# Kernel tuning notes

Hardware: AMD Instinct MI355X
Metric: run time of the kernel (lower is better)

The kernel has to match this reference:

```python
import jax, jax.numpy as jnp
import numpy as np
import math

B, S, D = 4, 2048, 1024
N_HEADS = 16
D_FF = 4096
T_DIM = 256
KEEP_RATIO = 0.7
EPS = 1e-5


def _layernorm(x):
    mu = jnp.mean(x, axis=-1, keepdims=True)
    var = jnp.mean((x - mu) ** 2, axis=-1, keepdims=True)
    return (x - mu) * jax.lax.rsqrt(var + EPS)


def _ada_ln(x, cond, W, b):
    # cond: (B, T_DIM); W: (2D, T_DIM)
    p = jax.nn.silu(cond) @ W.T + b            # (B, 2D)
    gamma, beta = jnp.split(p, 2, axis=-1)
    return _layernorm(x) * (1.0 + gamma[:, None, :]) + beta[:, None, :]


def _mha(h, in_w, in_b, out_w, out_b):
    b, s, d = h.shape
    hd = d // N_HEADS
    qkv = h @ in_w.T + in_b                     # (b, s, 3d)
    q, k, v = jnp.split(qkv, 3, axis=-1)
    def heads(t):
        return t.reshape(b, s, N_HEADS, hd).transpose(0, 2, 1, 3)
    q, k, v = heads(q), heads(k), heads(v)
    scores = jnp.einsum('bhqd,bhkd->bhqk', q, k) / math.sqrt(hd)
    attn = jax.nn.softmax(scores, axis=-1)
    o = jnp.einsum('bhqk,bhkd->bhqd', attn, v)  # (b, h, s, hd)
    o = o.transpose(0, 2, 1, 3).reshape(b, s, d)
    return o @ out_w.T + out_b


def setup_inputs() -> dict:
    key = jax.random.key(0)
    ks = jax.random.split(key, 24)
    sc = 0.02
    return {
        'x': jax.random.normal(ks[0], (B, S, D), jnp.float32),
        't_emb': jax.random.normal(ks[1], (B, T_DIM), jnp.float32),
        'tr_w1': jax.random.normal(ks[2], (32, D), jnp.float32) * sc,
        'tr_b1': jnp.zeros((32,), jnp.float32),
        'tr_w2': jax.random.normal(ks[3], (1, 32), jnp.float32) * sc,
        'tr_b2': jnp.zeros((1,), jnp.float32),
        'ln1_w': jax.random.normal(ks[4], (2 * D, T_DIM), jnp.float32) * sc,
        'ln1_b': jnp.zeros((2 * D,), jnp.float32),
        'ln2_w': jax.random.normal(ks[5], (2 * D, T_DIM), jnp.float32) * sc,
        'ln2_b': jnp.zeros((2 * D,), jnp.float32),
        'in_proj_w': jax.random.normal(ks[6], (3 * D, D), jnp.float32) * sc,
        'in_proj_b': jnp.zeros((3 * D,), jnp.float32),
        'out_w': jax.random.normal(ks[7], (D, D), jnp.float32) * sc,
        'out_b': jnp.zeros((D,), jnp.float32),
        'ffn_w1': jax.random.normal(ks[8], (D_FF, D), jnp.float32) * sc,
        'ffn_b1': jnp.zeros((D_FF,), jnp.float32),
        'ffn_w2': jax.random.normal(ks[9], (D, D_FF), jnp.float32) * sc,
        'ffn_b2': jnp.zeros((D,), jnp.float32),
        # torch inits gates to zero; use small randn so the block is non-trivial
        'gate_attn': jax.random.normal(ks[10], (1, 1, D), jnp.float32) * sc,
        'gate_ffn': jax.random.normal(ks[11], (1, 1, D), jnp.float32) * sc,
    }


def reference(x, t_emb, tr_w1, tr_b1, tr_w2, tr_b2, ln1_w, ln1_b, ln2_w, ln2_b,
              in_proj_w, in_proj_b, out_w, out_b, ffn_w1, ffn_b1, ffn_w2, ffn_b2,
              gate_attn, gate_ffn):
    b, s, d = x.shape
    num_keep = max(int(s * KEEP_RATIO), 1)

    # token importance on detached x (stop_gradient mirrors x.detach())
    xd = jax.lax.stop_gradient(x)
    imp = jax.nn.silu(xd @ tr_w1.T + tr_b1) @ tr_w2.T + tr_b2  # (b, s, 1)
    imp = imp[..., 0]
    _, idx = jax.lax.top_k(imp, num_keep)
    idx = jnp.sort(idx, axis=-1)                               # (b, num_keep)

    x_sel = jnp.take_along_axis(x, idx[..., None], axis=1)     # (b, k, d)

    h = _ada_ln(x_sel, t_emb, ln1_w, ln1_b)
    h = _mha(h, in_proj_w, in_proj_b, out_w, out_b)
    x_sel = x_sel + gate_attn * h

    h = _ada_ln(x_sel, t_emb, ln2_w, ln2_b)
    h = jax.nn.gelu(h @ ffn_w1.T + ffn_b1, approximate=False) @ ffn_w2.T + ffn_b2
    x_sel = x_sel + gate_ffn * h

    batch_idx = jnp.arange(b)[:, None]
    return x.at[batch_idx, idx].set(x_sel)
```

## Files before the change

### kernel.cpp

```cpp
#include <hip/hip_runtime.h>
#include <hip/hip_bf16.h>
#include <cmath>
#include <cstdint>

typedef __bf16 bf16;
typedef __bf16 bf16x8 __attribute__((ext_vector_type(8)));
typedef __bf16 bf16x4 __attribute__((ext_vector_type(4)));
typedef float  f32x4  __attribute__((ext_vector_type(4)));

constexpr int B_   = 4;
constexpr int S_   = 2048;
constexpr int D_   = 1024;
constexpr int H_   = 16;
constexpr int DFF_ = 4096;
constexpr int TD_  = 256;
constexpr int KEEP = 1433;
constexpr int M_TOT = B_ * KEEP;
constexpr int MPAD  = 5888;
constexpr int QT64  = (KEEP + 63) / 64;
constexpr int NKV   = (KEEP + 63) / 64;
constexpr float EPS = 1e-5f;
constexpr float QSCALE = 0.18033688011112042f;

__device__ __forceinline__ f32x4 mfma16(bf16x8 a, bf16x8 b, f32x4 c) {
  return __builtin_amdgcn_mfma_f32_16x16x32_bf16(a, b, c, 0, 0, 0);
}

#define GLOAD_LDS(gp, lp)                                                     \
  __builtin_amdgcn_global_load_lds(                                           \
      (const __attribute__((address_space(1))) void*)(gp),                    \
      (__attribute__((address_space(3))) void*)(lp), 16, 0, 0)

__global__ __launch_bounds__(256) void k_impgemv(
    const float* __restrict__ x, const float* __restrict__ w1,
    double* __restrict__ hidden)
{
  const int lane = threadIdx.x & 63, w = threadIdx.x >> 6;
  const int tok0 = blockIdx.x * 16 + w * 4;
  const int u0 = blockIdx.y * 8;
  const float* xb = x + (size_t)tok0 * D_ + lane * 4;
  const float* wb = w1 + (size_t)u0 * D_ + lane * 4;
  double acc[4][8] = {};
#pragma unroll 2
  for (int c = 0; c < D_; c += 256) {
    float4 xv[4], wv[8];
#pragma unroll
    for (int i = 0; i < 4; ++i)
      xv[i] = *(const float4*)(xb + (size_t)i * D_ + c);
#pragma unroll
    for (int u = 0; u < 8; ++u)
      wv[u] = *(const float4*)(wb + (size_t)u * D_ + c);
#pragma unroll
    for (int i = 0; i < 4; ++i)
#pragma unroll
      for (int u = 0; u < 8; ++u) {
        acc[i][u] += (double)xv[i].x * (double)wv[u].x;
        acc[i][u] += (double)xv[i].y * (double)wv[u].y;
        acc[i][u] += (double)xv[i].z * (double)wv[u].z;
        acc[i][u] += (double)xv[i].w * (double)wv[u].w;
      }
  }
#pragma unroll
  for (int i = 0; i < 4; ++i)
#pragma unroll
    for (int u = 0; u < 8; ++u) {
      double s = acc[i][u];
      for (int o = 32; o > 0; o >>= 1) s += __shfl_xor(s, o);
      acc[i][u] = s;
    }
  if (lane == 0) {
#pragma unroll
    for (int i = 0; i < 4; ++i)
#pragma unroll
      for (int u = 0; u < 8; ++u)
        hidden[(size_t)(tok0 + i) * 32 + u0 + u] = acc[i][u];
  }
}

__global__ __launch_bounds__(256) void k_imptail(
    const double* __restrict__ hidden, const float* __restrict__ b1,
    const float* __restrict__ w2, const float* __restrict__ b2,
    double* __restrict__ imp)
{
  const int tok = blockIdx.x * 256 + threadIdx.x;
  const double* hp = hidden + (size_t)tok * 32;
  double r = 0.0;
#pragma unroll
  for (int u = 0; u < 32; ++u) {
    double s = hp[u] + (double)b1[u];
    double sv = s / (1.0 + exp(-s));
    r += sv * (double)w2[u];
  }
  imp[tok] = r + (double)b2[0];
}

__global__ __launch_bounds__(256) void k_rank(const double* __restrict__ imp,
                                              int* __restrict__ rank)
{
  const int b = blockIdx.x >> 5;
  const int seg = blockIdx.x & 31;
  __shared__ double vals[S_];
  const double* ib = imp + (size_t)b * S_;
  for (int i = threadIdx.x; i < S_ / 2; i += 256)
    ((double2*)vals)[i] = ((const double2*)ib)[i];
  __syncthreads();
  const int tl = threadIdx.x >> 2;
  const int part = threadIdx.x & 3;
  const int s = seg * 64 + tl;
  const double v = vals[s];
  int cnt = 0;
  for (int j = part * 512; j < (part + 1) * 512; ++j) {
    double u = vals[j];
    cnt += (u > v) || (u == v && j < s);
  }
  cnt += __shfl_xor(cnt, 1);
  cnt += __shfl_xor(cnt, 2);
  if (part == 0) rank[b * S_ + s] = cnt;
}

__global__ __launch_bounds__(256) void k_compact(const int* __restrict__ rank,
                                                 int* __restrict__ idx)
{
  const int b = blockIdx.x;
  __shared__ int wcnt[4];
  __shared__ int base_s;
  if (threadIdx.x == 0) base_s = 0;
  __syncthreads();
  const int t = threadIdx.x, lane = t & 63, w = t >> 6;
  for (int c = 0; c < S_ / 256; ++c) {
    const int s = c * 256 + t;
    const bool kept = rank[b * S_ + s] < KEEP;
    unsigned long long m = __ballot(kept);
    int piw = __popcll(m & ((1ull << lane) - 1ull));
    if (lane == 0) wcnt[w] = __popcll(m);
    __syncthreads();
    int off = base_s;
    for (int i = 0; i < w; ++i) off += wcnt[i];
    if (kept) idx[b * KEEP + off + piw] = s;
    __syncthreads();
    if (t == 0) base_s += wcnt[0] + wcnt[1] + wcnt[2] + wcnt[3];
    __syncthreads();
  }
}

__global__ __launch_bounds__(256) void k_condproj(
    const float* __restrict__ temb, const float* __restrict__ W,
    const float* __restrict__ bias, float* __restrict__ p)
{
  const int gw = (int)((blockIdx.x * 256 + threadIdx.x) >> 6);
  const int lane = threadIdx.x & 63;
  const int b = gw >> 11;
  const int row = gw & 2047;
  const float* te = temb + (size_t)b * TD_;
  const float* wr = W + (size_t)row * TD_;
  float acc = 0.f;
  for (int i = lane; i < TD_; i += 64) {
    float c = te[i];
    acc += (c / (1.f + __expf(-c))) * wr[i];
  }
  for (int o = 32; o > 0; o >>= 1) acc += __shfl_down(acc, o);
  if (lane == 0) p[(size_t)b * 2 * D_ + row] = acc + bias[row];
}

__global__ void k_f2b(const float* __restrict__ src, bf16* __restrict__ dst, int n4)
{
  int i = blockIdx.x * 256 + threadIdx.x;
  if (i < n4) {
    float4 v = ((const float4*)src)[i];
    bf16x4 o = {(bf16)v.x, (bf16)v.y, (bf16)v.z, (bf16)v.w};
    ((bf16x4*)dst)[i] = o;
  }
}

__global__ __launch_bounds__(256) void k_adaln(
    const float* __restrict__ xsrc, const int* __restrict__ idx,
    const float* __restrict__ p, bf16* __restrict__ hout)
{
  const int r = blockIdx.x, t = threadIdx.x;
  bf16* orow = hout + (size_t)r * D_;
  if (r >= M_TOT) {
    bf16x4 z = {(bf16)0.f, (bf16)0.f, (bf16)0.f, (bf16)0.f};
    ((bf16x4*)orow)[t] = z;
    return;
  }
  const int b = r / KEEP, j = r - b * KEEP;
  const int s = idx[b * KEEP + j];
  const float* xr = xsrc + ((size_t)(b * S_ + s)) * D_;
  float4 v = ((const float4*)xr)[t];
  __shared__ float red[8];
  float sum = v.x + v.y + v.z + v.w;
  for (int o = 32; o > 0; o >>= 1) sum += __shfl_down(sum, o);
  const int lane = t & 63, w = t >> 6;
  if (lane == 0) red[w] = sum;
  __syncthreads();
  const float mu = (red[0] + red[1] + red[2] + red[3]) * (1.f / D_);
  const float dx = v.x - mu, dy = v.y - mu, dz = v.z - mu, dw = v.w - mu;
  float vs = dx * dx + dy * dy + dz * dz + dw * dw;
  for (int o = 32; o > 0; o >>= 1) vs += __shfl_down(vs, o);
  if (lane == 0) red[4 + w] = vs;
  __syncthreads();
  const float rstd = rsqrtf((red[4] + red[5] + red[6] + red[7]) * (1.f / D_) + EPS);
  const float* gp = p + (size_t)b * 2 * D_;
  float4 g  = ((const float4*)gp)[t];
  float4 be = ((const float4*)(gp + D_))[t];
  bf16x4 o;
  o[0] = (bf16)(dx * rstd * (1.f + g.x) + be.x);
  o[1] = (bf16)(dy * rstd * (1.f + g.y) + be.y);
  o[2] = (bf16)(dz * rstd * (1.f + g.z) + be.z);
  o[3] = (bf16)(dw * rstd * (1.f + g.w) + be.w);
  ((bf16x4*)orow)[t] = o;
}

template <int BN, int MODE>
__global__ __launch_bounds__(256) void k_gemm(
    const bf16* __restrict__ A, const bf16* __restrict__ W,
    const float* __restrict__ bias, bf16* __restrict__ Cbf,
    const float* __restrict__ gate, const int* __restrict__ idx,
    float* __restrict__ resid, int N, int K, int gn)
{
  constexpr int WN = BN / 2;
  constexpr int NJ = WN / 16;
  __shared__ bf16 As[2][128 * 64];
  __shared__ bf16 Ws[2][BN * 64];
  const int t = threadIdx.x, lane = t & 63;
  const int w = t >> 6, wr = w >> 1, wc = w & 1;
  const int fr = lane & 15, fq = lane >> 4;

  const int nwg = gridDim.x, orig = blockIdx.x;
  const int q8 = nwg >> 3, r8 = nwg & 7;
  const int xc = orig & 7, pos = orig >> 3;
  const int wgid = (xc < r8 ? xc * (q8 + 1) : r8 * (q8 + 1) + (xc - r8) * q8) + pos;
  const int bm = wgid / gn, bn = wgid - bm * gn;

  const bf16* Ab = A + (size_t)bm * 128 * K;
  const bf16* Wb = W + (size_t)bn * BN * K;

  auto stage = [&](int buf, int kt) {
    const int ko = kt * 64;
#pragma unroll
    for (int it = 0; it < 4; ++it) {
      const int e = it * 256 + t;
      const int row = e >> 3, pc = e & 7;
      const int lc = pc ^ (row & 7);
      GLOAD_LDS(Ab + (size_t)row * K + ko + lc * 8, &As[buf][0] + e * 8);
    }
#pragma unroll
    for (int it = 0; it < BN / 32; ++it) {
      const int e = it * 256 + t;
      const int row = e >> 3, pc = e & 7;
      const int lc = pc ^ (row & 7);
      GLOAD_LDS(Wb + (size_t)row * K + ko + lc * 8, &Ws[buf][0] + e * 8);
    }
  };

  f32x4 acc[4][NJ] = {};
  stage(0, 0);
  const int nkt = K >> 6;
  int cur = 0;
  for (int kt = 0; kt < nkt; ++kt) {
    __syncthreads();
    if (kt + 1 < nkt) stage(cur ^ 1, kt + 1);
    const char* Al = (const char*)&As[cur][0];
    const char* Wl = (const char*)&Ws[cur][0];
#pragma unroll
    for (int kk = 0; kk < 2; ++kk) {
      bf16x8 af[4], wf[NJ];
#pragma unroll
      for (int i = 0; i < 4; ++i)
        af[i] = *(const bf16x8*)(Al + (wr * 64 + i * 16 + fr) * 128 +
                                 (((kk * 4 + fq) ^ (fr & 7)) << 4));
#pragma unroll
      for (int j = 0; j < NJ; ++j)
        wf[j] = *(const bf16x8*)(Wl + (wc * WN + j * 16 + fr) * 128 +
                                 (((kk * 4 + fq) ^ (fr & 7)) << 4));
#pragma unroll
      for (int i = 0; i < 4; ++i)
#pragma unroll
        for (int j = 0; j < NJ; ++j)
          acc[i][j] = mfma16(af[i], wf[j], acc[i][j]);
    }
    cur ^= 1;
  }

#pragma unroll
  for (int i = 0; i < 4; ++i) {
#pragma unroll
    for (int j = 0; j < NJ; ++j) {
#pragma unroll
      for (int r = 0; r < 4; ++r) {
        const int m = bm * 128 + wr * 64 + i * 16 + fq * 4 + r;
        const int n = bn * BN + wc * WN + j * 16 + fr;
        float v = acc[i][j][r] + bias[n];
        if (MODE == 0) {
          if (n < D_) v *= QSCALE;
          Cbf[(size_t)m * N + n] = (bf16)v;
        } else if (MODE == 1) {
          float gl = 0.5f * v * (1.f + erff(v * 0.70710678118654752f));
          Cbf[(size_t)m * N + n] = (bf16)gl;
        } else {
          if (m < M_TOT) {
            const int b = m / KEEP, jj = m - b * KEEP;
            const int s = idx[b * KEEP + jj];
            resid[((size_t)(b * S_ + s)) * D_ + n] += gate[n] * v;
          }
        }
      }
    }
  }
}

__global__ __launch_bounds__(256) void k_attn(const bf16* __restrict__ qkv,
                                              bf16* __restrict__ out)
{
  __shared__ bf16 Klds[2][64 * 64];
  __shared__ bf16 Vlds[2][64 * 64];

  const int t = threadIdx.x;
  const int lane = t & 63, w = t >> 6;
  const int fr = lane & 15, fq = lane >> 4;
  const int qt = blockIdx.x, h = blockIdx.y, b = blockIdx.z;
  const size_t rowbase = (size_t)b * KEEP;
  const size_t RS = 3 * D_;
  const bf16* kbase = qkv + rowbase * RS + D_ + h * 64;
  const bf16* vbase = qkv + rowbase * RS + 2 * D_ + h * 64;

  const int wq0 = qt * 64 + w * 16;
  const int qrow = min(wq0 + fr, KEEP - 1);
  const bf16* qp = qkv + (rowbase + qrow) * RS + h * 64 + fq * 8;
  const bf16x8 qf0 = *(const bf16x8*)qp;
  const bf16x8 qf1 = *(const bf16x8*)(qp + 32);

  f32x4 o[4] = {};
  float mrow = -INFINITY, lrow = 0.f;

  const int p0 = t, p1 = 256 + t;
  auto kaddr = [&](int p, int kv) {
    const int row = p >> 3, c8p = p & 7;
    const int c8 = c8p ^ ((row & 7) ^ (row >> 3));
    const int gr = min(kv + row, KEEP - 1);
    return kbase + (size_t)gr * RS + c8 * 8;
  };
  auto vaddr = [&](int p, int kv) {
    const int db = p >> 7, ksub = (p >> 3) & 15, jr = (p >> 1) & 3,
              c8lo = p & 1;
    const int vrow = ksub * 4 + jr, vc8 = db * 2 + c8lo;
    const int gr = min(kv + vrow, KEEP - 1);
    return vbase + (size_t)gr * RS + vc8 * 8;
  };
  const bf16* kp0 = kaddr(p0, 0);
  const bf16* kp1 = kaddr(p1, 0);
  const bf16* vp0 = vaddr(p0, 0);
  const bf16* vp1 = vaddr(p1, 0);

  auto stage_fast = [&](int buf) {
    GLOAD_LDS(kp0, &Klds[buf][0] + p0 * 8);
    GLOAD_LDS(kp1, &Klds[buf][0] + p1 * 8);
    GLOAD_LDS(vp0, &Vlds[buf][0] + p0 * 8);
    GLOAD_LDS(vp1, &Vlds[buf][0] + p1 * 8);
    kp0 += 64 * RS; kp1 += 64 * RS; vp0 += 64 * RS; vp1 += 64 * RS;
  };
  auto stage_last = [&](int buf, int kv) {
    GLOAD_LDS(kaddr(p0, kv), &Klds[buf][0] + p0 * 8);
    GLOAD_LDS(kaddr(p1, kv), &Klds[buf][0] + p1 * 8);
    GLOAD_LDS(vaddr(p0, kv), &Vlds[buf][0] + p0 * 8);
    GLOAD_LDS(vaddr(p1, kv), &Vlds[buf][0] + p1 * 8);
  };

  stage_fast(0);
  int cur = 0;

  const unsigned vbase_lds0 =
      (unsigned)(size_t)(__attribute__((address_space(3))) bf16*)&Vlds[0][0];
  const unsigned vbase_lds1 =
      (unsigned)(size_t)(__attribute__((address_space(3))) bf16*)&Vlds[1][0];

  for (int ti = 0; ti < NKV; ++ti) {
    const int kv = ti * 64;
    __syncthreads();
    if (ti < NKV - 2) stage_fast(cur ^ 1);
    else if (ti == NKV - 2) stage_last(cur ^ 1, kv + 64);

    const char* Kl = (const char*)&Klds[cur][0];

    f32x4 sc[4];
    __builtin_amdgcn_s_setprio(1);
#pragma unroll
    for (int f = 0; f < 4; ++f) {
      const int row = ((f >> 1) << 5) + ((fr >> 2) << 3) + ((f & 1) << 1) +
                      (fr & 1) + (((fr >> 1) & 1) << 2);
      const int swz = (row & 7) ^ (row >> 3);
      const bf16x8 kf0 = *(const bf16x8*)(Kl + row * 128 + ((fq ^ swz) << 4));
      const bf16x8 kf1 =
          *(const bf16x8*)(Kl + row * 128 + (((fq ^ 4) ^ swz) << 4));
      f32x4 s = {0.f, 0.f, 0.f, 0.f};
      s = mfma16(kf0, qf0, s);
      s = mfma16(kf1, qf1, s);
      sc[f] = s;
    }
    __builtin_amdgcn_s_setprio(0);

    if (ti == NKV - 1) {
#pragma unroll
      for (int f = 0; f < 4; ++f)
#pragma unroll
        for (int r = 0; r < 4; ++r) {
          const int kl = ((f >> 1) << 5) + (fq << 3) + ((f & 1) << 1) +
                         (r & 1) + ((r >> 1) << 2);
          if (kv + kl >= KEEP) sc[f][r] = -INFINITY;
        }
    }
    float mx = sc[0][0];
#pragma unroll
    for (int f = 0; f < 4; ++f)
#pragma unroll
      for (int r = 0; r < 4; ++r) mx = fmaxf(mx, sc[f][r]);
    mx = fmaxf(mx, __shfl_xor(mx, 16));
    mx = fmaxf(mx, __shfl_xor(mx, 32));

    const bool noresc = __all(mx <= mrow + 8.f);
    const float mnew = noresc ? mrow : fmaxf(mrow, mx);
    float ps = 0.f;
    bf16 pe[4][4];
#pragma unroll
    for (int f = 0; f < 4; ++f)
#pragma unroll
      for (int r = 0; r < 4; ++r) {
        const float pv = exp2f(sc[f][r] - mnew);
        ps += pv;
        pe[f][r] = (bf16)pv;
      }
    ps += __shfl_xor(ps, 16);
    ps += __shfl_xor(ps, 32);
    if (!noresc) {
      const float fac = exp2f(mrow - mnew);
      lrow *= fac;
#pragma unroll
      for (int db = 0; db < 4; ++db) {
        o[db][0] *= fac; o[db][1] *= fac; o[db][2] *= fac; o[db][3] *= fac;
      }
      mrow = mnew;
    }
    lrow += ps;

    const bf16x8 pb[2] = {
        {pe[0][0], pe[0][1], pe[1][0], pe[1][1],
         pe[0][2], pe[0][3], pe[1][2], pe[1][3]},
        {pe[2][0], pe[2][1], pe[3][0], pe[3][1],
         pe[2][2], pe[2][3], pe[3][2], pe[3][3]}};
    const unsigned vb =
        (cur ? vbase_lds1 : vbase_lds0) + ((unsigned)fq << 7);
#pragma unroll
    for (int c = 0; c < 2; ++c) {
      const unsigned addr = vb + c * 1024;
      bf16x4 t0, t1, t2, t3, t4, t5, t6, t7;
      asm volatile(
          "ds_read_b64_tr_b16 %0, %8 offset:0\n\t"
          "ds_read_b64_tr_b16 %1, %8 offset:128\n\t"
          "ds_read_b64_tr_b16 %2, %8 offset:2048\n\t"
          "ds_read_b64_tr_b16 %3, %8 offset:2176\n\t"
          "ds_read_b64_tr_b16 %4, %8 offset:4096\n\t"
          "ds_read_b64_tr_b16 %5, %8 offset:4224\n\t"
          "ds_read_b64_tr_b16 %6, %8 offset:6144\n\t"
          "ds_read_b64_tr_b16 %7, %8 offset:6272\n\t"
          "s_waitcnt lgkmcnt(0)"
          : "=&v"(t0), "=&v"(t1), "=&v"(t2), "=&v"(t3),
            "=&v"(t4), "=&v"(t5), "=&v"(t6), "=&v"(t7)
          : "v"(addr));
      const bf16x8 vf0 = __builtin_shufflevector(t0, t1, 0, 1, 2, 3, 4, 5, 6, 7);
      const bf16x8 vf1 = __builtin_shufflevector(t2, t3, 0, 1, 2, 3, 4, 5, 6, 7);
      const bf16x8 vf2 = __builtin_shufflevector(t4, t5, 0, 1, 2, 3, 4, 5, 6, 7);
      const bf16x8 vf3 = __builtin_shufflevector(t6, t7, 0, 1, 2, 3, 4, 5, 6, 7);
      __builtin_amdgcn_s_setprio(1);
      o[0] = mfma16(vf0, pb[c], o[0]);
      o[1] = mfma16(vf1, pb[c], o[1]);
      o[2] = mfma16(vf2, pb[c], o[2]);
      o[3] = mfma16(vf3, pb[c], o[3]);
      __builtin_amdgcn_s_setprio(0);
    }
    cur ^= 1;
  }

  const int q = wq0 + fr;
  if (q < KEEP) {
    const float inv = 1.f / lrow;
#pragma unroll
    for (int db = 0; db < 4; ++db) {
      bf16x4 wv = {(bf16)(o[db][0] * inv), (bf16)(o[db][1] * inv),
                   (bf16)(o[db][2] * inv), (bf16)(o[db][3] * inv)};
      *(bf16x4*)(out + (rowbase + q) * (size_t)D_ + h * 64 + db * 16 + fq * 4) =
          wv;
    }
  }
}

extern "C" void kernel_launch(void* const* d_in, const int* in_sizes, int n_in,
                              void* d_out, int out_size, void* d_ws, size_t ws_size,
                              hipStream_t stream)
{
  (void)in_sizes; (void)n_in; (void)out_size; (void)ws_size;
  const float* x      = (const float*)d_in[0];
  const float* t_emb  = (const float*)d_in[1];
  const float* tr_w1  = (const float*)d_in[2];
  const float* tr_b1  = (const float*)d_in[3];
  const float* tr_w2  = (const float*)d_in[4];
  const float* tr_b2  = (const float*)d_in[5];
  const float* ln1_w  = (const float*)d_in[6];
  const float* ln1_b  = (const float*)d_in[7];
  const float* ln2_w  = (const float*)d_in[8];
  const float* ln2_b  = (const float*)d_in[9];
  const float* in_w   = (const float*)d_in[10];
  const float* in_b   = (const float*)d_in[11];
  const float* out_w  = (const float*)d_in[12];
  const float* out_b  = (const float*)d_in[13];
  const float* f1_w   = (const float*)d_in[14];
  const float* f1_b   = (const float*)d_in[15];
  const float* f2_w   = (const float*)d_in[16];
  const float* f2_b   = (const float*)d_in[17];
  const float* gate_a = (const float*)d_in[18];
  const float* gate_f = (const float*)d_in[19];

  char* ws = (char*)d_ws;
  size_t off = 0;
  auto alloc = [&](size_t bytes) -> char* {
    char* p = ws + off;
    off = (off + bytes + 255) & ~(size_t)255;
    return p;
  };
  double* imp  = (double*)alloc((size_t)B_ * S_ * 8);
  double* hid  = (double*)alloc((size_t)B_ * S_ * 32 * 8);
  int* rank    = (int*)alloc((size_t)B_ * S_ * 4);
  int* idx     = (int*)alloc((size_t)B_ * KEEP * 4);
  float* p1    = (float*)alloc((size_t)B_ * 2 * D_ * 4);
  float* p2    = (float*)alloc((size_t)B_ * 2 * D_ * 4);
  bf16* w_in   = (bf16*)alloc((size_t)3 * D_ * D_ * 2);
  bf16* w_out  = (bf16*)alloc((size_t)D_ * D_ * 2);
  bf16* w_f1   = (bf16*)alloc((size_t)DFF_ * D_ * 2);
  bf16* w_f2   = (bf16*)alloc((size_t)D_ * DFF_ * 2);
  bf16* h_bf   = (bf16*)alloc((size_t)MPAD * D_ * 2);
  bf16* big    = (bf16*)alloc((size_t)MPAD * (3 * D_ + D_) * 2);
  bf16* qkv    = big;
  bf16* attn   = big + (size_t)MPAD * 3 * D_;
  bf16* ffn1   = big;

  hipMemcpyAsync(d_out, x, (size_t)B_ * S_ * D_ * 4, hipMemcpyDeviceToDevice, stream);

  k_impgemv<<<dim3(B_ * S_ / 16, 4), 256, 0, stream>>>(x, tr_w1, hid);
  k_imptail<<<B_ * S_ / 256, 256, 0, stream>>>(hid, tr_b1, tr_w2, tr_b2, imp);
  k_rank<<<B_ * 32, 256, 0, stream>>>(imp, rank);
  k_compact<<<B_, 256, 0, stream>>>(rank, idx);

  k_condproj<<<(B_ * 2 * D_) / 4, 256, 0, stream>>>(t_emb, ln1_w, ln1_b, p1);
  k_condproj<<<(B_ * 2 * D_) / 4, 256, 0, stream>>>(t_emb, ln2_w, ln2_b, p2);

  k_f2b<<<(3 * D_ * D_ / 4 + 255) / 256, 256, 0, stream>>>(in_w, w_in, 3 * D_ * D_ / 4);
  k_f2b<<<(D_ * D_ / 4 + 255) / 256, 256, 0, stream>>>(out_w, w_out, D_ * D_ / 4);
  k_f2b<<<(DFF_ * D_ / 4 + 255) / 256, 256, 0, stream>>>(f1_w, w_f1, DFF_ * D_ / 4);
  k_f2b<<<(DFF_ * D_ / 4 + 255) / 256, 256, 0, stream>>>(f2_w, w_f2, DFF_ * D_ / 4);

  k_adaln<<<MPAD, 256, 0, stream>>>(x, idx, p1, h_bf);
  k_gemm<128, 0><<<46 * 24, 256, 0, stream>>>(
      h_bf, w_in, in_b, qkv, nullptr, nullptr, nullptr, 3 * D_, D_, 24);
  k_attn<<<dim3(QT64, H_, B_), 256, 0, stream>>>(qkv, attn);
  k_gemm<64, 2><<<46 * 16, 256, 0, stream>>>(
      attn, w_out, out_b, nullptr, gate_a, idx, (float*)d_out, D_, D_, 16);
  k_adaln<<<MPAD, 256, 0, stream>>>((const float*)d_out, idx, p2, h_bf);
  k_gemm<128, 1><<<46 * 32, 256, 0, stream>>>(
      h_bf, w_f1, f1_b, ffn1, nullptr, nullptr, nullptr, DFF_, D_, 32);
  k_gemm<64, 2><<<46 * 16, 256, 0, stream>>>(
      ffn1, w_f2, f2_b, nullptr, gate_f, idx, (float*)d_out, D_, DFF_, 16);
}
```

Before: 458.3 us.

## Process two query groups per wave in attention to reuse K/V tiles

Each attention block now covers 128 query rows instead of 64, with every wave computing two 16-row query groups against each staged K/V tile. This halves K/V staging and LDS reads per query and gives more independent MFMAs per tile. In exchange it doubles accumulator registers and halves the number of blocks, which can lower occupancy and worsen load balance across CUs.

```diff
diff --git a/kernel.cpp b/kernel.cpp
--- a/kernel.cpp
+++ b/kernel.cpp
@@ -17,7 +17,7 @@
 constexpr int KEEP = 1433;
 constexpr int M_TOT = B_ * KEEP;
 constexpr int MPAD  = 5888;
-constexpr int QT64  = (KEEP + 63) / 64;
+constexpr int QT128 = (KEEP + 127) / 128;
 constexpr int NKV   = (KEEP + 63) / 64;
 constexpr float EPS = 1e-5f;
 constexpr float QSCALE = 0.18033688011112042f;
@@ -324,14 +324,19 @@
   const bf16* kbase = qkv + rowbase * RS + D_ + h * 64;
   const bf16* vbase = qkv + rowbase * RS + 2 * D_ + h * 64;
 
-  const int wq0 = qt * 64 + w * 16;
-  const int qrow = min(wq0 + fr, KEEP - 1);
-  const bf16* qp = qkv + (rowbase + qrow) * RS + h * 64 + fq * 8;
-  const bf16x8 qf0 = *(const bf16x8*)qp;
-  const bf16x8 qf1 = *(const bf16x8*)(qp + 32);
-
-  f32x4 o[4] = {};
-  float mrow = -INFINITY, lrow = 0.f;
+  const int wq0 = qt * 128 + w * 32;
+  bf16x8 qf[2][2];
+#pragma unroll
+  for (int g = 0; g < 2; ++g) {
+    const int qrow = min(wq0 + g * 16 + fr, KEEP - 1);
+    const bf16* qp = qkv + (rowbase + qrow) * RS + h * 64 + fq * 8;
+    qf[g][0] = *(const bf16x8*)qp;
+    qf[g][1] = *(const bf16x8*)(qp + 32);
+  }
+
+  f32x4 o[2][4] = {};
+  float mrow[2] = {-INFINITY, -INFINITY};
+  float lrow[2] = {0.f, 0.f};
 
   const int p0 = t, p1 = 256 + t;
   auto kaddr = [&](int p, int kv) {
@@ -382,7 +387,7 @@
 
     const char* Kl = (const char*)&Klds[cur][0];
 
-    f32x4 sc[4];
+    f32x4 sc[2][4];
     __builtin_amdgcn_s_setprio(1);
 #pragma unroll
     for (int f = 0; f < 4; ++f) {
@@ -392,10 +397,13 @@
       const bf16x8 kf0 = *(const bf16x8*)(Kl + row * 128 + ((fq ^ swz) << 4));
       const bf16x8 kf1 =
           *(const bf16x8*)(Kl + row * 128 + (((fq ^ 4) ^ swz) << 4));
-      f32x4 s = {0.f, 0.f, 0.f, 0.f};
-      s = mfma16(kf0, qf0, s);
-      s = mfma16(kf1, qf1, s);
-      sc[f] = s;
+#pragma unroll
+      for (int g = 0; g < 2; ++g) {
+        f32x4 s = {0.f, 0.f, 0.f, 0.f};
+        s = mfma16(kf0, qf[g][0], s);
+        s = mfma16(kf1, qf[g][1], s);
+        sc[g][f] = s;
+      }
     }
     __builtin_amdgcn_s_setprio(0);
 
@@ -406,47 +414,57 @@
         for (int r = 0; r < 4; ++r) {
           const int kl = ((f >> 1) << 5) + (fq << 3) + ((f & 1) << 1) +
                          (r & 1) + ((r >> 1) << 2);
-          if (kv + kl >= KEEP) sc[f][r] = -INFINITY;
+          if (kv + kl >= KEEP) {
+            sc[0][f][r] = -INFINITY;
+            sc[1][f][r] = -INFINITY;
+          }
         }
     }
-    float mx = sc[0][0];
-#pragma unroll
-    for (int f = 0; f < 4; ++f)
-#pragma unroll
-      for (int r = 0; r < 4; ++r) mx = fmaxf(mx, sc[f][r]);
-    mx = fmaxf(mx, __shfl_xor(mx, 16));
-    mx = fmaxf(mx, __shfl_xor(mx, 32));
-
-    const bool noresc = __all(mx <= mrow + 8.f);
-    const float mnew = noresc ? mrow : fmaxf(mrow, mx);
-    float ps = 0.f;
-    bf16 pe[4][4];
-#pragma unroll
-    for (int f = 0; f < 4; ++f)
-#pragma unroll
-      for (int r = 0; r < 4; ++r) {
-        const float pv = exp2f(sc[f][r] - mnew);
-        ps += pv;
-        pe[f][r] = (bf16)pv;
+    bf16 pe[2][4][4];
+#pragma unroll
+    for (int g = 0; g < 2; ++g) {
+      float mx = sc[g][0][0];
+#pragma unroll
+      for (int f = 0; f < 4; ++f)
+#pragma unroll
+        for (int r = 0; r < 4; ++r) mx = fmaxf(mx, sc[g][f][r]);
+      mx = fmaxf(mx, __shfl_xor(mx, 16));
+      mx = fmaxf(mx, __shfl_xor(mx, 32));
+      const bool noresc = __all(mx <= mrow[g] + 8.f);
+      const float mnew = noresc ? mrow[g] : fmaxf(mrow[g], mx);
+      float ps = 0.f;
+#pragma unroll
+      for (int f = 0; f < 4; ++f)
+#pragma unroll
+        for (int r = 0; r < 4; ++r) {
+          const float pv = exp2f(sc[g][f][r] - mnew);
+          ps += pv;
+          pe[g][f][r] = (bf16)pv;
+        }
+      ps += __shfl_xor(ps, 16);
+      ps += __shfl_xor(ps, 32);
+      if (!noresc) {
+        const float fac = exp2f(mrow[g] - mnew);
+        lrow[g] *= fac;
+#pragma unroll
+        for (int db = 0; db < 4; ++db) {
+          o[g][db][0] *= fac; o[g][db][1] *= fac;
+          o[g][db][2] *= fac; o[g][db][3] *= fac;
+        }
+        mrow[g] = mnew;
       }
-    ps += __shfl_xor(ps, 16);
-    ps += __shfl_xor(ps, 32);
-    if (!noresc) {
-      const float fac = exp2f(mrow - mnew);
-      lrow *= fac;
-#pragma unroll
-      for (int db = 0; db < 4; ++db) {
-        o[db][0] *= fac; o[db][1] *= fac; o[db][2] *= fac; o[db][3] *= fac;
-      }
-      mrow = mnew;
-    }
-    lrow += ps;
-
-    const bf16x8 pb[2] = {
-        {pe[0][0], pe[0][1], pe[1][0], pe[1][1],
-         pe[0][2], pe[0][3], pe[1][2], pe[1][3]},
-        {pe[2][0], pe[2][1], pe[3][0], pe[3][1],
-         pe[2][2], pe[2][3], pe[3][2], pe[3][3]}};
+      lrow[g] += ps;
+    }
+
+    const bf16x8 pb[2][2] = {
+        {{pe[0][0][0], pe[0][0][1], pe[0][1][0], pe[0][1][1],
+          pe[0][0][2], pe[0][0][3], pe[0][1][2], pe[0][1][3]},
+         {pe[0][2][0], pe[0][2][1], pe[0][3][0], pe[0][3][1],
+          pe[0][2][2], pe[0][2][3], pe[0][3][2], pe[0][3][3]}},
+        {{pe[1][0][0], pe[1][0][1], pe[1][1][0], pe[1][1][1],
+          pe[1][0][2], pe[1][0][3], pe[1][1][2], pe[1][1][3]},
+         {pe[1][2][0], pe[1][2][1], pe[1][3][0], pe[1][3][1],
+          pe[1][2][2], pe[1][2][3], pe[1][3][2], pe[1][3][3]}}};
     const unsigned vb =
         (cur ? vbase_lds1 : vbase_lds0) + ((unsigned)fq << 7);
 #pragma unroll
@@ -471,24 +489,30 @@
       const bf16x8 vf2 = __builtin_shufflevector(t4, t5, 0, 1, 2, 3, 4, 5, 6, 7);
       const bf16x8 vf3 = __builtin_shufflevector(t6, t7, 0, 1, 2, 3, 4, 5, 6, 7);
       __builtin_amdgcn_s_setprio(1);
-      o[0] = mfma16(vf0, pb[c], o[0]);
-      o[1] = mfma16(vf1, pb[c], o[1]);
-      o[2] = mfma16(vf2, pb[c], o[2]);
-      o[3] = mfma16(vf3, pb[c], o[3]);
+#pragma unroll
+      for (int g = 0; g < 2; ++g) {
+        o[g][0] = mfma16(vf0, pb[g][c], o[g][0]);
+        o[g][1] = mfma16(vf1, pb[g][c], o[g][1]);
+        o[g][2] = mfma16(vf2, pb[g][c], o[g][2]);
+        o[g][3] = mfma16(vf3, pb[g][c], o[g][3]);
+      }
       __builtin_amdgcn_s_setprio(0);
     }
     cur ^= 1;
   }
 
-  const int q = wq0 + fr;
-  if (q < KEEP) {
-    const float inv = 1.f / lrow;
-#pragma unroll
-    for (int db = 0; db < 4; ++db) {
-      bf16x4 wv = {(bf16)(o[db][0] * inv), (bf16)(o[db][1] * inv),
-                   (bf16)(o[db][2] * inv), (bf16)(o[db][3] * inv)};
-      *(bf16x4*)(out + (rowbase + q) * (size_t)D_ + h * 64 + db * 16 + fq * 4) =
-          wv;
+#pragma unroll
+  for (int g = 0; g < 2; ++g) {
+    const int q = wq0 + g * 16 + fr;
+    if (q < KEEP) {
+      const float inv = 1.f / lrow[g];
+#pragma unroll
+      for (int db = 0; db < 4; ++db) {
+        bf16x4 wv = {(bf16)(o[g][db][0] * inv), (bf16)(o[g][db][1] * inv),
+                     (bf16)(o[g][db][2] * inv), (bf16)(o[g][db][3] * inv)};
+        *(bf16x4*)(out + (rowbase + q) * (size_t)D_ + h * 64 + db * 16 +
+                   fq * 4) = wv;
+      }
     }
   }
 }
@@ -560,7 +584,7 @@
   k_adaln<<<MPAD, 256, 0, stream>>>(x, idx, p1, h_bf);
   k_gemm<128, 0><<<46 * 24, 256, 0, stream>>>(
       h_bf, w_in, in_b, qkv, nullptr, nullptr, nullptr, 3 * D_, D_, 24);
-  k_attn<<<dim3(QT64, H_, B_), 256, 0, stream>>>(qkv, attn);
+  k_attn<<<dim3(QT128, H_, B_), 256, 0, stream>>>(qkv, attn);
   k_gemm<64, 2><<<46 * 16, 256, 0, stream>>>(
       attn, w_out, out_b, nullptr, gate_a, idx, (float*)d_out, D_, D_, 16);
   k_adaln<<<MPAD, 256, 0, stream>>>((const float*)d_out, idx, p2, h_bf);
```

New measurement: 471.2 us. 2.8% more time.
